# Performance work log

Measured on AMD Instinct MI355X. Metric: run time of the kernel, lower is better.

The kernel has to match this reference:

```python
import jax, jax.numpy as jnp
import numpy as np

N_NODES = 100000
N_EDGES = 1600000
IN_CH = 128
HIDDEN = 64
N_CLASSES = 40


def setup_inputs() -> dict:
    key = jax.random.key(0)
    k_x, k_e, k_w1, k_w2 = jax.random.split(key, 4)
    x = jax.random.normal(k_x, (N_NODES, IN_CH), dtype=jnp.float32)
    edge_index = jax.random.randint(k_e, (2, N_EDGES), 0, N_NODES, dtype=jnp.int64)
    # Glorot-style init for GCN weights
    W1 = jax.random.normal(k_w1, (IN_CH, HIDDEN), dtype=jnp.float32) * (1.0 / np.sqrt(IN_CH))
    b1 = jnp.zeros((HIDDEN,), dtype=jnp.float32)
    W2 = jax.random.normal(k_w2, (HIDDEN, N_CLASSES), dtype=jnp.float32) * (1.0 / np.sqrt(HIDDEN))
    b2 = jnp.zeros((N_CLASSES,), dtype=jnp.float32)
    return {"x": x, "edge_index": edge_index, "W1": W1, "b1": b1, "W2": W2, "b2": b2}


def reference(x, edge_index, W1, b1, W2, b2):
    n = x.shape[0]
    # PyG GCNConv: add self-loops, symmetric degree normalization
    loop = jnp.arange(n, dtype=edge_index.dtype)
    src = jnp.concatenate([edge_index[0], loop])  # message sources j
    dst = jnp.concatenate([edge_index[1], loop])  # aggregation targets i
    w = jnp.ones(src.shape[0], dtype=x.dtype)     # edge_weight=None -> ones
    deg = jax.ops.segment_sum(w, dst, num_segments=n)
    dinv = jnp.where(deg > 0, jax.lax.rsqrt(jnp.maximum(deg, 1e-12)), 0.0)
    norm = dinv[src] * dinv[dst]                  # [E+N]

    def gcn_conv(h, W, b):
        hw = h @ W                                # transform first (fewer flops)
        msg = hw[src] * norm[:, None]             # gather + normalize
        return jax.ops.segment_sum(msg, dst, num_segments=n) + b  # scatter-add

    h = jax.nn.relu(gcn_conv(x, W1, b1))
    # dropout is identity in eval mode
    out = gcn_conv(h, W2, b2)
    return out
```

## Files before the change

kernel.cpp:

```cpp
#include <hip/hip_runtime.h>
#include <hip/hip_bf16.h>

#define NNODES 100000
#define NEDGES 1600000
#define IN_CH 128
#define HID 64
#define NC 40
#define NPAD 100352
#define NBUK 196
#define CAP 9216
#define BCHUNK 4096
#define NBIN 391

typedef unsigned short ushort_t;
typedef unsigned int uint_t;
typedef __attribute__((ext_vector_type(8))) short short8;
typedef __attribute__((ext_vector_type(4))) float floatx4;
typedef __attribute__((ext_vector_type(2))) float f32x2;

__device__ __forceinline__ ushort_t f2bf(float f) {
    union { float ff; unsigned int i; } t;
    t.ff = f;
    unsigned int r = t.i + 0x7fff + ((t.i >> 16) & 1);
    return (ushort_t)(r >> 16);
}
__device__ __forceinline__ void acc2(f32x2& a, uint_t p) {
    union { unsigned int i; float f; } lo, hi;
    lo.i = p << 16;
    hi.i = p & 0xffff0000u;
    f32x2 v = {lo.f, hi.f};
    a += v;
}

__global__ __launch_bounds__(256) void k_bin0(
    const int* __restrict__ srcs, const int* __restrict__ dsts,
    int* __restrict__ gcur, uint_t* __restrict__ tmp, int e,
    const float* __restrict__ W1, ushort_t* __restrict__ Wp,
    ushort_t* __restrict__ hb, int n)
{
    __shared__ uint_t pk[BCHUNK];
    __shared__ ushort_t bk[BCHUNK];
    __shared__ uint_t spk[BCHUNK];
    __shared__ ushort_t sb[BCHUNK];
    __shared__ int hist[NBUK];
    __shared__ int lscan[NBUK];
    __shared__ int base[NBUK];
    __shared__ int sc2[256];
    int t = threadIdx.x;
    if (blockIdx.x >= NBIN) {
        for (int i = t; i < IN_CH * HID; i += 256) {
            int j = i & 7;
            int m = (i >> 3) & 15;
            int ct = (i >> 7) & 3;
            int quad = (i >> 9) & 3;
            int kc = i >> 11;
            int k = kc * 32 + quad * 8 + j;
            int c = ct * 16 + m;
            Wp[i] = f2bf(W1[k * HID + c]);
        }
        uint_t* hbz = (uint_t*)(hb + (size_t)n * HID);
        if (t < 32) hbz[t] = 0;
        return;
    }
    int begin = blockIdx.x * BCHUNK;
    int cnt = e - begin; if (cnt > BCHUNK) cnt = BCHUNK;

    for (int i = t; i < NBUK; i += 256) hist[i] = 0;
    __syncthreads();
    for (int j = t; j < cnt; j += 256) {
        int d = dsts[begin + j];
        int s = srcs[begin + j];
        int b = d >> 9;
        pk[j] = (uint_t)s | ((uint_t)(d & 511) << 17);
        bk[j] = (ushort_t)b;
        atomicAdd(&hist[b], 1);
    }
    __syncthreads();
    int c = (t < NBUK) ? hist[t] : 0;
    sc2[t] = c;
    __syncthreads();
    for (int off = 1; off < 256; off <<= 1) {
        int v = (t >= off) ? sc2[t - off] : 0;
        __syncthreads();
        sc2[t] += v;
        __syncthreads();
    }
    if (t < NBUK) {
        lscan[t] = sc2[t] - c;
        base[t] = t * CAP + atomicAdd(&gcur[t], c);
        hist[t] = 0;
    }
    __syncthreads();
    for (int j = t; j < cnt; j += 256) {
        int b = bk[j];
        int r = atomicAdd(&hist[b], 1);
        int slot = lscan[b] + r;
        spk[slot] = pk[j];
        sb[slot] = (ushort_t)b;
    }
    __syncthreads();
    for (int j = t; j < cnt; j += 256) {
        int b = sb[j];
        int pos = base[b] + (j - lscan[b]);
        if (pos < (b + 1) * CAP) tmp[pos] = spk[j];
    }
}

__global__ __launch_bounds__(256) void k_sort(
    const uint_t* __restrict__ tmp, const int* __restrict__ gcur,
    int* __restrict__ row_start, float* __restrict__ dinv,
    uint_t* __restrict__ es, int n, int e)
{
    __shared__ int cnt[512];
    __shared__ int sc[512];
    __shared__ int red[256];
    __shared__ uint_t esl[CAP];
    int t = threadIdx.x;
    int b = blockIdx.x;
    int d0 = b << 9;
    int total = gcur[b];
    if (total > CAP) total = CAP;
    int part = 0;
    for (int i = t; i < b; i += 256) part += gcur[i];
    red[t] = part;
    cnt[t] = 0; cnt[t + 256] = 0;
    __syncthreads();
    for (int off = 128; off > 0; off >>= 1) {
        if (t < off) red[t] += red[t + off];
        __syncthreads();
    }
    int gb = red[0];
    const uint_t* seg = tmp + b * CAP;
    for (int j = t; j < total; j += 256)
        atomicAdd(&cnt[seg[j] >> 17], 1);
    __syncthreads();
    sc[t] = cnt[t]; sc[t + 256] = cnt[t + 256];
    __syncthreads();
    for (int off = 1; off < 512; off <<= 1) {
        int v0 = (t >= off) ? sc[t - off] : 0;
        int i1 = t + 256;
        int v1 = (i1 >= off) ? sc[i1 - off] : 0;
        __syncthreads();
        sc[t] += v0; sc[i1] += v1;
        __syncthreads();
    }
#pragma unroll
    for (int q = 0; q < 2; ++q) {
        int i = t + q * 256;
        int node = d0 + i;
        int start = gb + sc[i] - cnt[i];
        if (node < n) {
            row_start[node] = start;
            dinv[node] = rsqrtf((float)cnt[i] + 1.0f);
        }
        cnt[i] = start - gb;
    }
    __syncthreads();
    for (int j = t; j < total; j += 256) {
        uint_t p = seg[j];
        int ld = (int)(p >> 17);
        int pos = atomicAdd(&cnt[ld], 1);
        esl[pos] = p & 0x1FFFFu;
    }
    __syncthreads();
    for (int j = t; j < total; j += 256) es[gb + j] = esl[j];
    if (b == NBUK - 1 && t == 0) row_start[n] = e;
}

__global__ __launch_bounds__(256) void k_gemm1(
    const float* __restrict__ x, const ushort_t* __restrict__ Wp,
    const float* __restrict__ dinv, ushort_t* __restrict__ hw1, int n)
{
    int wave = threadIdx.x >> 6;
    int lane = threadIdx.x & 63;
    int m = lane & 15;
    int quad = lane >> 4;
    int row = blockIdx.x * 64 + wave * 16 + m;
    int rowc = row < n ? row : (n - 1);
    const float* xr = x + (size_t)rowc * IN_CH + quad * 8;

    floatx4 acc[4];
#pragma unroll
    for (int ct = 0; ct < 4; ++ct) acc[ct] = (floatx4){0.f, 0.f, 0.f, 0.f};

#pragma unroll
    for (int kc = 0; kc < 4; ++kc) {
        float4 xa = *(const float4*)(xr + kc * 32);
        float4 xb = *(const float4*)(xr + kc * 32 + 4);
        short8 a;
        a[0] = (short)f2bf(xa.x); a[1] = (short)f2bf(xa.y);
        a[2] = (short)f2bf(xa.z); a[3] = (short)f2bf(xa.w);
        a[4] = (short)f2bf(xb.x); a[5] = (short)f2bf(xb.y);
        a[6] = (short)f2bf(xb.z); a[7] = (short)f2bf(xb.w);
#pragma unroll
        for (int ct = 0; ct < 4; ++ct) {
            short8 b = *(const short8*)(Wp + ((((kc * 4 + quad) * 4 + ct) * 16 + m) << 3));
            acc[ct] = __builtin_amdgcn_mfma_f32_16x16x32_bf16(a, b, acc[ct], 0, 0, 0);
        }
    }
    int r0 = blockIdx.x * 64 + wave * 16 + quad * 4;
#pragma unroll
    for (int r = 0; r < 4; ++r) {
        int rr = r0 + r;
        if (rr < n) {
            float di = dinv[rr];
            ushort_t* o = hw1 + (size_t)rr * HID + m;
#pragma unroll
            for (int ct = 0; ct < 4; ++ct) o[ct * 16] = f2bf(acc[ct][r] * di);
        } else if (rr == n) {
            ushort_t* o = hw1 + (size_t)n * HID + m;
#pragma unroll
            for (int ct = 0; ct < 4; ++ct) o[ct * 16] = 0;
        }
    }
}

__global__ __launch_bounds__(256, 4) void k_agg1(
    const int* __restrict__ row_start, const uint_t* __restrict__ es,
    const float* __restrict__ dinv, const uint_t* __restrict__ hw1u,
    const float* __restrict__ b1, ushort_t* __restrict__ hb, int n)
{
    int lane = threadIdx.x & 63;
    int obase = lane & 56;
    int ol = lane & 7;
    int node = blockIdx.x * 32 + (threadIdx.x >> 3);
    bool valid = node < n;
    int rs = valid ? row_start[node] : 0;
    int re = valid ? row_start[node + 1] : 0;
    float di = valid ? dinv[node] : 0.f;
    int selfrow = valid ? node : n;

    f32x2 c0, c1, c2, c3;
    {
        uint4 sp = *(const uint4*)(hw1u + (size_t)selfrow * 32 + ol * 4);
        c0 = (f32x2){0.f, 0.f}; c1 = c0; c2 = c0; c3 = c0;
        acc2(c0, sp.x); acc2(c1, sp.y); acc2(c2, sp.z); acc2(c3, sp.w);
    }
    int el = n;
    if (rs < re) {
        int idx = rs + ol;
        el = (idx < re) ? (int)es[idx] : n;
    }
    for (int base = rs; base < re; base += 8) {
        int el_cur = el;
        int nb = base + 8;
        if (nb < re) {
            int idx = nb + ol;
            el = (idx < re) ? (int)es[idx] : n;
        }
        uint4 p[8];
#pragma unroll
        for (int b = 0; b < 8; ++b) {
            int s = __shfl(el_cur, obase + b);
            p[b] = *(const uint4*)(hw1u + (size_t)s * 32 + ol * 4);
        }
#pragma unroll
        for (int b = 0; b < 8; ++b) {
            acc2(c0, p[b].x); acc2(c1, p[b].y);
            acc2(c2, p[b].z); acc2(c3, p[b].w);
        }
    }
    if (valid) {
        float4 bb0 = ((const float4*)b1)[ol * 2];
        float4 bb1 = ((const float4*)b1)[ol * 2 + 1];
        float h0 = fmaxf(c0.x * di + bb0.x, 0.f);
        float h1 = fmaxf(c0.y * di + bb0.y, 0.f);
        float h2 = fmaxf(c1.x * di + bb0.z, 0.f);
        float h3 = fmaxf(c1.y * di + bb0.w, 0.f);
        float h4 = fmaxf(c2.x * di + bb1.x, 0.f);
        float h5 = fmaxf(c2.y * di + bb1.y, 0.f);
        float h6 = fmaxf(c3.x * di + bb1.z, 0.f);
        float h7 = fmaxf(c3.y * di + bb1.w, 0.f);
        uint4 st;
        st.x = (uint_t)f2bf(h0 * di) | ((uint_t)f2bf(h1 * di) << 16);
        st.y = (uint_t)f2bf(h2 * di) | ((uint_t)f2bf(h3 * di) << 16);
        st.z = (uint_t)f2bf(h4 * di) | ((uint_t)f2bf(h5 * di) << 16);
        st.w = (uint_t)f2bf(h6 * di) | ((uint_t)f2bf(h7 * di) << 16);
        *(uint4*)(hb + (size_t)node * HID + ol * 8) = st;
    }
}

__global__ __launch_bounds__(256, 4) void k_agg2(
    const int* __restrict__ row_start, const uint_t* __restrict__ es,
    const float* __restrict__ dinv, const uint_t* __restrict__ hbu,
    const float* __restrict__ W2, const float* __restrict__ b2,
    float* __restrict__ out, int n)
{
    __shared__ float wsm[HID * NC];
    __shared__ float hsm[32][68];
    for (int i = threadIdx.x; i < HID * NC; i += 256) wsm[i] = W2[i];
    __syncthreads();

    int lane = threadIdx.x & 63;
    int obase = lane & 56;
    int ol = lane & 7;
    int slot = threadIdx.x >> 3;
    int node = blockIdx.x * 32 + slot;
    bool valid = node < n;
    int rs = valid ? row_start[node] : 0;
    int re = valid ? row_start[node + 1] : 0;
    float di = valid ? dinv[node] : 0.f;
    int selfrow = valid ? node : n;

    f32x2 c0, c1, c2, c3;
    {
        uint4 sp = *(const uint4*)(hbu + (size_t)selfrow * 32 + ol * 4);
        c0 = (f32x2){0.f, 0.f}; c1 = c0; c2 = c0; c3 = c0;
        acc2(c0, sp.x); acc2(c1, sp.y); acc2(c2, sp.z); acc2(c3, sp.w);
    }
    int el = n;
    if (rs < re) {
        int idx = rs + ol;
        el = (idx < re) ? (int)es[idx] : n;
    }
    for (int base = rs; base < re; base += 8) {
        int el_cur = el;
        int nb = base + 8;
        if (nb < re) {
            int idx = nb + ol;
            el = (idx < re) ? (int)es[idx] : n;
        }
        uint4 p[8];
#pragma unroll
        for (int b = 0; b < 8; ++b) {
            int s = __shfl(el_cur, obase + b);
            p[b] = *(const uint4*)(hbu + (size_t)s * 32 + ol * 4);
        }
#pragma unroll
        for (int b = 0; b < 8; ++b) {
            acc2(c0, p[b].x); acc2(c1, p[b].y);
            acc2(c2, p[b].z); acc2(c3, p[b].w);
        }
    }
    {
        float4 g0, g1;
        g0.x = c0.x * di; g0.y = c0.y * di; g0.z = c1.x * di; g0.w = c1.y * di;
        g1.x = c2.x * di; g1.y = c2.y * di; g1.z = c3.x * di; g1.w = c3.y * di;
        *(float4*)&hsm[slot][ol * 8] = g0;
        *(float4*)&hsm[slot][ol * 8 + 4] = g1;
    }
    int w8 = (threadIdx.x >> 6) * 8;
    int qm = lane >> 4;
    int lq = lane & 15;
    int lw = (lq < 10) ? lq : 0;
    const float4* w4 = (const float4*)wsm;
#pragma unroll
    for (int pass = 0; pass < 2; ++pass) {
        int slot2 = w8 + pass * 4 + qm;
        int node2 = blockIdx.x * 32 + slot2;
        float4 acc = ((const float4*)b2)[lw];
#pragma unroll 4
        for (int k4 = 0; k4 < 16; ++k4) {
            float4 hk = *(const float4*)&hsm[slot2][k4 * 4];
            float4 w0 = w4[(k4 * 4 + 0) * 10 + lw];
            float4 w1 = w4[(k4 * 4 + 1) * 10 + lw];
            float4 w2 = w4[(k4 * 4 + 2) * 10 + lw];
            float4 w3 = w4[(k4 * 4 + 3) * 10 + lw];
            acc.x += hk.x * w0.x + hk.y * w1.x + hk.z * w2.x + hk.w * w3.x;
            acc.y += hk.x * w0.y + hk.y * w1.y + hk.z * w2.y + hk.w * w3.y;
            acc.z += hk.x * w0.z + hk.y * w1.z + hk.z * w2.z + hk.w * w3.z;
            acc.w += hk.x * w0.w + hk.y * w1.w + hk.z * w2.w + hk.w * w3.w;
        }
        if (node2 < n && lq < 10)
            *(float4*)(out + (size_t)node2 * NC + lq * 4) = acc;
    }
}

extern "C" void kernel_launch(void* const* d_in, const int* in_sizes, int n_in,
                              void* d_out, int out_size, void* d_ws, size_t ws_size,
                              hipStream_t stream) {
    const float* x  = (const float*)d_in[0];
    const int* edge = (const int*)d_in[1];
    const float* W1 = (const float*)d_in[2];
    const float* b1 = (const float*)d_in[3];
    const float* W2 = (const float*)d_in[4];
    const float* b2 = (const float*)d_in[5];
    float* out      = (float*)d_out;

    const int n = in_sizes[0] / IN_CH;
    const int e = in_sizes[1] / 2;
    const int* srcs = edge;
    const int* dsts = edge + e;

    int*      gcur      = (int*)d_ws;
    int*      row_start = gcur + 256;
    float*    dinv      = (float*)(row_start + NPAD);
    uint_t*   tmp       = (uint_t*)(dinv + NPAD);
    uint_t*   es        = tmp + (size_t)NBUK * CAP;
    ushort_t* Wp        = (ushort_t*)(es + NEDGES);
    ushort_t* hw1       = Wp + 8192;
    ushort_t* hb        = hw1 + (size_t)(NNODES + 1) * HID;

    hipMemsetAsync(gcur, 0, NBUK * sizeof(int), stream);
    k_bin0<<<NBIN + 1, 256, 0, stream>>>(srcs, dsts, gcur, tmp, e, W1, Wp, hb, n);
    k_sort<<<NBUK, 256, 0, stream>>>(tmp, gcur, row_start, dinv, es, n, e);
    k_gemm1<<<(n + 63) / 64, 256, 0, stream>>>(x, Wp, dinv, hw1, n);
    k_agg1<<<(n + 31) / 32, 256, 0, stream>>>(row_start, es, dinv, (const uint_t*)hw1, b1, hb, n);
    k_agg2<<<(n + 31) / 32, 256, 0, stream>>>(row_start, es, dinv, (const uint_t*)hb, W2, b2, out, n);
}
```

Before: 211.2 us.

## Fuse all GCN stages into one persistent cooperative kernel with grid syncs

Merges binning, bucket sort, GEMM1, and both aggregation stages into a single cooperative kernel of 1024 persistent blocks, separated by grid-wide barriers and sharing a unioned LDS buffer. The aim is to remove per-kernel launch gaps and tail drain between stages. The binning chunk size is reduced so the LDS union fits four blocks per CU. In exchange, the aggregation stages run with fewer resident blocks looping over tiles and pay grid-sync costs, with a fallback to the separate kernels if the cooperative launch fails.

```diff
diff --git a/kernel.cpp b/kernel.cpp
--- a/kernel.cpp
+++ b/kernel.cpp
@@ -1,5 +1,8 @@
 #include <hip/hip_runtime.h>
 #include <hip/hip_bf16.h>
+#include <hip/hip_cooperative_groups.h>
+
+namespace cg = cooperative_groups;
 
 #define NNODES 100000
 #define NEDGES 1600000
@@ -9,8 +12,8 @@
 #define NPAD 100352
 #define NBUK 196
 #define CAP 9216
-#define BCHUNK 4096
-#define NBIN 391
+#define BCH 2560
+#define GRID 1024
 
 typedef unsigned short ushort_t;
 typedef unsigned int uint_t;
@@ -32,157 +35,153 @@
     a += v;
 }
 
-__global__ __launch_bounds__(256) void k_bin0(
+struct SmBin {
+    uint_t pk[BCH]; ushort_t bk[BCH];
+    uint_t spk[BCH]; ushort_t sb[BCH];
+    int hist[NBUK]; int lscan[NBUK]; int base[NBUK]; int sc2[256];
+};
+struct SmSortScan { int sc[512]; int red[256]; };
+struct SmSort { int cnt[512]; union { SmSortScan s; uint_t esl[CAP]; } u; };
+struct SmG2 { float wsm[HID * NC]; float hsm[32][68]; };
+union Sm { SmBin bin; SmSort sort; SmG2 g2; };
+static_assert(sizeof(Sm) <= 39936, "LDS budget for 4 blocks/CU");
+
+
+__device__ __forceinline__ void side_work(const float* __restrict__ W1,
+                                          ushort_t* __restrict__ Wp,
+                                          ushort_t* __restrict__ hb, int n, int t) {
+    for (int i = t; i < IN_CH * HID; i += 256) {
+        int j = i & 7;
+        int m = (i >> 3) & 15;
+        int ct = (i >> 7) & 3;
+        int quad = (i >> 9) & 3;
+        int kc = i >> 11;
+        int k = kc * 32 + quad * 8 + j;
+        int c = ct * 16 + m;
+        Wp[i] = f2bf(W1[k * HID + c]);
+    }
+    uint_t* hbz = (uint_t*)(hb + (size_t)n * HID);
+    if (t < 32) hbz[t] = 0;
+}
+
+__device__ __forceinline__ void bin_chunk(SmBin& sm, int chunk,
     const int* __restrict__ srcs, const int* __restrict__ dsts,
-    int* __restrict__ gcur, uint_t* __restrict__ tmp, int e,
-    const float* __restrict__ W1, ushort_t* __restrict__ Wp,
-    ushort_t* __restrict__ hb, int n)
-{
-    __shared__ uint_t pk[BCHUNK];
-    __shared__ ushort_t bk[BCHUNK];
-    __shared__ uint_t spk[BCHUNK];
-    __shared__ ushort_t sb[BCHUNK];
-    __shared__ int hist[NBUK];
-    __shared__ int lscan[NBUK];
-    __shared__ int base[NBUK];
-    __shared__ int sc2[256];
-    int t = threadIdx.x;
-    if (blockIdx.x >= NBIN) {
-        for (int i = t; i < IN_CH * HID; i += 256) {
-            int j = i & 7;
-            int m = (i >> 3) & 15;
-            int ct = (i >> 7) & 3;
-            int quad = (i >> 9) & 3;
-            int kc = i >> 11;
-            int k = kc * 32 + quad * 8 + j;
-            int c = ct * 16 + m;
-            Wp[i] = f2bf(W1[k * HID + c]);
-        }
-        uint_t* hbz = (uint_t*)(hb + (size_t)n * HID);
-        if (t < 32) hbz[t] = 0;
-        return;
-    }
-    int begin = blockIdx.x * BCHUNK;
-    int cnt = e - begin; if (cnt > BCHUNK) cnt = BCHUNK;
-
-    for (int i = t; i < NBUK; i += 256) hist[i] = 0;
-    __syncthreads();
-    for (int j = t; j < cnt; j += 256) {
+    int* __restrict__ gcur, uint_t* __restrict__ tmp, int e, int t)
+{
+    int begin = chunk * BCH;
+    int ec = e - begin; if (ec > BCH) ec = BCH;
+    for (int i = t; i < NBUK; i += 256) sm.hist[i] = 0;
+    __syncthreads();
+    for (int j = t; j < ec; j += 256) {
         int d = dsts[begin + j];
         int s = srcs[begin + j];
         int b = d >> 9;
-        pk[j] = (uint_t)s | ((uint_t)(d & 511) << 17);
-        bk[j] = (ushort_t)b;
-        atomicAdd(&hist[b], 1);
-    }
-    __syncthreads();
-    int c = (t < NBUK) ? hist[t] : 0;
-    sc2[t] = c;
+        sm.pk[j] = (uint_t)s | ((uint_t)(d & 511) << 17);
+        sm.bk[j] = (ushort_t)b;
+        atomicAdd(&sm.hist[b], 1);
+    }
+    __syncthreads();
+    int c = (t < NBUK) ? sm.hist[t] : 0;
+    sm.sc2[t] = c;
     __syncthreads();
     for (int off = 1; off < 256; off <<= 1) {
-        int v = (t >= off) ? sc2[t - off] : 0;
+        int v = (t >= off) ? sm.sc2[t - off] : 0;
         __syncthreads();
-        sc2[t] += v;
+        sm.sc2[t] += v;
         __syncthreads();
     }
     if (t < NBUK) {
-        lscan[t] = sc2[t] - c;
-        base[t] = t * CAP + atomicAdd(&gcur[t], c);
-        hist[t] = 0;
-    }
-    __syncthreads();
-    for (int j = t; j < cnt; j += 256) {
-        int b = bk[j];
-        int r = atomicAdd(&hist[b], 1);
-        int slot = lscan[b] + r;
-        spk[slot] = pk[j];
-        sb[slot] = (ushort_t)b;
-    }
-    __syncthreads();
-    for (int j = t; j < cnt; j += 256) {
-        int b = sb[j];
-        int pos = base[b] + (j - lscan[b]);
-        if (pos < (b + 1) * CAP) tmp[pos] = spk[j];
-    }
-}
-
-__global__ __launch_bounds__(256) void k_sort(
+        sm.lscan[t] = sm.sc2[t] - c;
+        sm.base[t] = t * CAP + atomicAdd(&gcur[t], c);
+        sm.hist[t] = 0;
+    }
+    __syncthreads();
+    for (int j = t; j < ec; j += 256) {
+        int b = sm.bk[j];
+        int r = atomicAdd(&sm.hist[b], 1);
+        int slot = sm.lscan[b] + r;
+        sm.spk[slot] = sm.pk[j];
+        sm.sb[slot] = (ushort_t)b;
+    }
+    __syncthreads();
+    for (int j = t; j < ec; j += 256) {
+        int b = sm.sb[j];
+        int pos = sm.base[b] + (j - sm.lscan[b]);
+        if (pos < (b + 1) * CAP) tmp[pos] = sm.spk[j];
+    }
+    __syncthreads();
+}
+
+__device__ __forceinline__ void sort_bucket(SmSort& sm, int b,
     const uint_t* __restrict__ tmp, const int* __restrict__ gcur,
     int* __restrict__ row_start, float* __restrict__ dinv,
-    uint_t* __restrict__ es, int n, int e)
-{
-    __shared__ int cnt[512];
-    __shared__ int sc[512];
-    __shared__ int red[256];
-    __shared__ uint_t esl[CAP];
-    int t = threadIdx.x;
-    int b = blockIdx.x;
+    uint_t* __restrict__ es, int n, int e, int t)
+{
     int d0 = b << 9;
     int total = gcur[b];
     if (total > CAP) total = CAP;
     int part = 0;
     for (int i = t; i < b; i += 256) part += gcur[i];
-    red[t] = part;
-    cnt[t] = 0; cnt[t + 256] = 0;
+    sm.u.s.red[t] = part;
+    sm.cnt[t] = 0; sm.cnt[t + 256] = 0;
     __syncthreads();
     for (int off = 128; off > 0; off >>= 1) {
-        if (t < off) red[t] += red[t + off];
+        if (t < off) sm.u.s.red[t] += sm.u.s.red[t + off];
         __syncthreads();
     }
-    int gb = red[0];
+    int gb = sm.u.s.red[0];
     const uint_t* seg = tmp + b * CAP;
     for (int j = t; j < total; j += 256)
-        atomicAdd(&cnt[seg[j] >> 17], 1);
-    __syncthreads();
-    sc[t] = cnt[t]; sc[t + 256] = cnt[t + 256];
+        atomicAdd(&sm.cnt[seg[j] >> 17], 1);
+    __syncthreads();
+    sm.u.s.sc[t] = sm.cnt[t]; sm.u.s.sc[t + 256] = sm.cnt[t + 256];
     __syncthreads();
     for (int off = 1; off < 512; off <<= 1) {
-        int v0 = (t >= off) ? sc[t - off] : 0;
+        int v0 = (t >= off) ? sm.u.s.sc[t - off] : 0;
         int i1 = t + 256;
-        int v1 = (i1 >= off) ? sc[i1 - off] : 0;
+        int v1 = (i1 >= off) ? sm.u.s.sc[i1 - off] : 0;
         __syncthreads();
-        sc[t] += v0; sc[i1] += v1;
+        sm.u.s.sc[t] += v0; sm.u.s.sc[i1] += v1;
         __syncthreads();
     }
 #pragma unroll
     for (int q = 0; q < 2; ++q) {
         int i = t + q * 256;
         int node = d0 + i;
-        int start = gb + sc[i] - cnt[i];
+        int start = gb + sm.u.s.sc[i] - sm.cnt[i];
         if (node < n) {
             row_start[node] = start;
-            dinv[node] = rsqrtf((float)cnt[i] + 1.0f);
-        }
-        cnt[i] = start - gb;
+            dinv[node] = rsqrtf((float)sm.cnt[i] + 1.0f);
+        }
+        sm.cnt[i] = start - gb;
     }
     __syncthreads();
     for (int j = t; j < total; j += 256) {
         uint_t p = seg[j];
         int ld = (int)(p >> 17);
-        int pos = atomicAdd(&cnt[ld], 1);
-        esl[pos] = p & 0x1FFFFu;
-    }
-    __syncthreads();
-    for (int j = t; j < total; j += 256) es[gb + j] = esl[j];
+        int pos = atomicAdd(&sm.cnt[ld], 1);
+        sm.u.esl[pos] = p & 0x1FFFFu;
+    }
+    __syncthreads();
+    for (int j = t; j < total; j += 256) es[gb + j] = sm.u.esl[j];
     if (b == NBUK - 1 && t == 0) row_start[n] = e;
-}
-
-__global__ __launch_bounds__(256) void k_gemm1(
+    __syncthreads();
+}
+
+__device__ __forceinline__ void gemm1_tile(int g,
     const float* __restrict__ x, const ushort_t* __restrict__ Wp,
-    const float* __restrict__ dinv, ushort_t* __restrict__ hw1, int n)
-{
-    int wave = threadIdx.x >> 6;
-    int lane = threadIdx.x & 63;
+    const float* __restrict__ dinv, ushort_t* __restrict__ hw1, int n, int t)
+{
+    int wave = t >> 6;
+    int lane = t & 63;
     int m = lane & 15;
     int quad = lane >> 4;
-    int row = blockIdx.x * 64 + wave * 16 + m;
+    int row = g * 64 + wave * 16 + m;
     int rowc = row < n ? row : (n - 1);
     const float* xr = x + (size_t)rowc * IN_CH + quad * 8;
-
     floatx4 acc[4];
 #pragma unroll
     for (int ct = 0; ct < 4; ++ct) acc[ct] = (floatx4){0.f, 0.f, 0.f, 0.f};
-
 #pragma unroll
     for (int kc = 0; kc < 4; ++kc) {
         float4 xa = *(const float4*)(xr + kc * 32);
@@ -194,11 +193,11 @@
         a[6] = (short)f2bf(xb.z); a[7] = (short)f2bf(xb.w);
 #pragma unroll
         for (int ct = 0; ct < 4; ++ct) {
-            short8 b = *(const short8*)(Wp + ((((kc * 4 + quad) * 4 + ct) * 16 + m) << 3));
-            acc[ct] = __builtin_amdgcn_mfma_f32_16x16x32_bf16(a, b, acc[ct], 0, 0, 0);
-        }
-    }
-    int r0 = blockIdx.x * 64 + wave * 16 + quad * 4;
+            short8 bfr = *(const short8*)(Wp + ((((kc * 4 + quad) * 4 + ct) * 16 + m) << 3));
+            acc[ct] = __builtin_amdgcn_mfma_f32_16x16x32_bf16(a, bfr, acc[ct], 0, 0, 0);
+        }
+    }
+    int r0 = g * 64 + wave * 16 + quad * 4;
 #pragma unroll
     for (int r = 0; r < 4; ++r) {
         int rr = r0 + r;
@@ -215,21 +214,20 @@
     }
 }
 
-__global__ __launch_bounds__(256, 4) void k_agg1(
+__device__ __forceinline__ void agg1_tile(int g,
     const int* __restrict__ row_start, const uint_t* __restrict__ es,
     const float* __restrict__ dinv, const uint_t* __restrict__ hw1u,
-    const float* __restrict__ b1, ushort_t* __restrict__ hb, int n)
-{
-    int lane = threadIdx.x & 63;
+    const float* __restrict__ b1, ushort_t* __restrict__ hb, int n, int t)
+{
+    int lane = t & 63;
     int obase = lane & 56;
     int ol = lane & 7;
-    int node = blockIdx.x * 32 + (threadIdx.x >> 3);
+    int node = g * 32 + (t >> 3);
     bool valid = node < n;
     int rs = valid ? row_start[node] : 0;
     int re = valid ? row_start[node + 1] : 0;
     float di = valid ? dinv[node] : 0.f;
     int selfrow = valid ? node : n;
-
     f32x2 c0, c1, c2, c3;
     {
         uint4 sp = *(const uint4*)(hw1u + (size_t)selfrow * 32 + ol * 4);
@@ -280,28 +278,21 @@
     }
 }
 
-__global__ __launch_bounds__(256, 4) void k_agg2(
+__device__ __forceinline__ void agg2_tile(SmG2& sm, int g,
     const int* __restrict__ row_start, const uint_t* __restrict__ es,
     const float* __restrict__ dinv, const uint_t* __restrict__ hbu,
-    const float* __restrict__ W2, const float* __restrict__ b2,
-    float* __restrict__ out, int n)
-{
-    __shared__ float wsm[HID * NC];
-    __shared__ float hsm[32][68];
-    for (int i = threadIdx.x; i < HID * NC; i += 256) wsm[i] = W2[i];
-    __syncthreads();
-
-    int lane = threadIdx.x & 63;
+    const float* __restrict__ b2, float* __restrict__ out, int n, int t)
+{
+    int lane = t & 63;
     int obase = lane & 56;
     int ol = lane & 7;
-    int slot = threadIdx.x >> 3;
-    int node = blockIdx.x * 32 + slot;
+    int slot = t >> 3;
+    int node = g * 32 + slot;
     bool valid = node < n;
     int rs = valid ? row_start[node] : 0;
     int re = valid ? row_start[node + 1] : 0;
     float di = valid ? dinv[node] : 0.f;
     int selfrow = valid ? node : n;
-
     f32x2 c0, c1, c2, c3;
     {
         uint4 sp = *(const uint4*)(hbu + (size_t)selfrow * 32 + ol * 4);
@@ -336,22 +327,22 @@
         float4 g0, g1;
         g0.x = c0.x * di; g0.y = c0.y * di; g0.z = c1.x * di; g0.w = c1.y * di;
         g1.x = c2.x * di; g1.y = c2.y * di; g1.z = c3.x * di; g1.w = c3.y * di;
-        *(float4*)&hsm[slot][ol * 8] = g0;
-        *(float4*)&hsm[slot][ol * 8 + 4] = g1;
-    }
-    int w8 = (threadIdx.x >> 6) * 8;
+        *(float4*)&sm.hsm[slot][ol * 8] = g0;
+        *(float4*)&sm.hsm[slot][ol * 8 + 4] = g1;
+    }
+    int w8 = (t >> 6) * 8;
     int qm = lane >> 4;
     int lq = lane & 15;
     int lw = (lq < 10) ? lq : 0;
-    const float4* w4 = (const float4*)wsm;
+    const float4* w4 = (const float4*)sm.wsm;
 #pragma unroll
     for (int pass = 0; pass < 2; ++pass) {
         int slot2 = w8 + pass * 4 + qm;
-        int node2 = blockIdx.x * 32 + slot2;
+        int node2 = g * 32 + slot2;
         float4 acc = ((const float4*)b2)[lw];
 #pragma unroll 4
         for (int k4 = 0; k4 < 16; ++k4) {
-            float4 hk = *(const float4*)&hsm[slot2][k4 * 4];
+            float4 hk = *(const float4*)&sm.hsm[slot2][k4 * 4];
             float4 w0 = w4[(k4 * 4 + 0) * 10 + lw];
             float4 w1 = w4[(k4 * 4 + 1) * 10 + lw];
             float4 w2 = w4[(k4 * 4 + 2) * 10 + lw];
@@ -364,6 +355,105 @@
         if (node2 < n && lq < 10)
             *(float4*)(out + (size_t)node2 * NC + lq * 4) = acc;
     }
+}
+
+extern "C" __global__ void __launch_bounds__(256, 4) k_all(
+    const int* __restrict__ srcs, const int* __restrict__ dsts,
+    int* __restrict__ gcur, uint_t* __restrict__ tmp,
+    const float* __restrict__ W1, ushort_t* __restrict__ Wp,
+    ushort_t* __restrict__ hb,
+    int* __restrict__ row_start, float* __restrict__ dinv,
+    uint_t* __restrict__ es,
+    const float* __restrict__ x, ushort_t* __restrict__ hw1,
+    const float* __restrict__ b1,
+    const float* __restrict__ W2, const float* __restrict__ b2,
+    float* __restrict__ out, int n, int e)
+{
+    __shared__ Sm sm;
+    cg::grid_group grid = cg::this_grid();
+    int t = threadIdx.x;
+    int nchunk = (e + BCH - 1) / BCH;
+
+    if ((int)blockIdx.x == nchunk) side_work(W1, Wp, hb, n, t);
+    for (int chunk = blockIdx.x; chunk < nchunk; chunk += GRID)
+        bin_chunk(sm.bin, chunk, srcs, dsts, gcur, tmp, e, t);
+    grid.sync();
+
+    for (int b = blockIdx.x; b < NBUK; b += GRID)
+        sort_bucket(sm.sort, b, tmp, gcur, row_start, dinv, es, n, e, t);
+    grid.sync();
+
+    {
+        int ng = (n + 63) >> 6;
+        for (int g = blockIdx.x; g < ng; g += GRID)
+            gemm1_tile(g, x, Wp, dinv, hw1, n, t);
+    }
+    grid.sync();
+
+    {
+        const uint_t* hw1u = (const uint_t*)hw1;
+        int nga = (n + 31) >> 5;
+        for (int g = blockIdx.x; g < nga; g += GRID)
+            agg1_tile(g, row_start, es, dinv, hw1u, b1, hb, n, t);
+    }
+    grid.sync();
+
+    {
+        const uint_t* hbu = (const uint_t*)hb;
+        for (int i = t; i < HID * NC; i += 256) sm.g2.wsm[i] = W2[i];
+        __syncthreads();
+        int nga = (n + 31) >> 5;
+        for (int g = blockIdx.x; g < nga; g += GRID)
+            agg2_tile(sm.g2, g, row_start, es, dinv, hbu, b2, out, n, t);
+    }
+}
+
+__global__ __launch_bounds__(256) void k_bin0(
+    const int* __restrict__ srcs, const int* __restrict__ dsts,
+    int* __restrict__ gcur, uint_t* __restrict__ tmp, int e,
+    const float* __restrict__ W1, ushort_t* __restrict__ Wp,
+    ushort_t* __restrict__ hb, int n)
+{
+    __shared__ SmBin smb;
+    int nchunk = (e + BCH - 1) / BCH;
+    if ((int)blockIdx.x >= nchunk) { side_work(W1, Wp, hb, n, threadIdx.x); return; }
+    bin_chunk(smb, blockIdx.x, srcs, dsts, gcur, tmp, e, threadIdx.x);
+}
+
+__global__ __launch_bounds__(256) void k_sort(
+    const uint_t* __restrict__ tmp, const int* __restrict__ gcur,
+    int* __restrict__ row_start, float* __restrict__ dinv,
+    uint_t* __restrict__ es, int n, int e)
+{
+    __shared__ SmSort sms;
+    sort_bucket(sms, blockIdx.x, tmp, gcur, row_start, dinv, es, n, e, threadIdx.x);
+}
+
+__global__ __launch_bounds__(256) void k_gemm1(
+    const float* __restrict__ x, const ushort_t* __restrict__ Wp,
+    const float* __restrict__ dinv, ushort_t* __restrict__ hw1, int n)
+{
+    gemm1_tile(blockIdx.x, x, Wp, dinv, hw1, n, threadIdx.x);
+}
+
+__global__ __launch_bounds__(256, 4) void k_agg1(
+    const int* __restrict__ row_start, const uint_t* __restrict__ es,
+    const float* __restrict__ dinv, const uint_t* __restrict__ hw1u,
+    const float* __restrict__ b1, ushort_t* __restrict__ hb, int n)
+{
+    agg1_tile(blockIdx.x, row_start, es, dinv, hw1u, b1, hb, n, threadIdx.x);
+}
+
+__global__ __launch_bounds__(256, 4) void k_agg2(
+    const int* __restrict__ row_start, const uint_t* __restrict__ es,
+    const float* __restrict__ dinv, const uint_t* __restrict__ hbu,
+    const float* __restrict__ W2, const float* __restrict__ b2,
+    float* __restrict__ out, int n)
+{
+    __shared__ SmG2 smg;
+    for (int i = threadIdx.x; i < HID * NC; i += 256) smg.wsm[i] = W2[i];
+    __syncthreads();
+    agg2_tile(smg, blockIdx.x, row_start, es, dinv, hbu, b2, out, n, threadIdx.x);
 }
 
 extern "C" void kernel_launch(void* const* d_in, const int* in_sizes, int n_in,
@@ -377,8 +467,8 @@
     const float* b2 = (const float*)d_in[5];
     float* out      = (float*)d_out;
 
-    const int n = in_sizes[0] / IN_CH;
-    const int e = in_sizes[1] / 2;
+    int n = in_sizes[0] / IN_CH;
+    int e = in_sizes[1] / 2;
     const int* srcs = edge;
     const int* dsts = edge + e;
 
@@ -391,10 +481,25 @@
     ushort_t* hw1       = Wp + 8192;
     ushort_t* hb        = hw1 + (size_t)(NNODES + 1) * HID;
 
-    hipMemsetAsync(gcur, 0, NBUK * sizeof(int), stream);
-    k_bin0<<<NBIN + 1, 256, 0, stream>>>(srcs, dsts, gcur, tmp, e, W1, Wp, hb, n);
-    k_sort<<<NBUK, 256, 0, stream>>>(tmp, gcur, row_start, dinv, es, n, e);
-    k_gemm1<<<(n + 63) / 64, 256, 0, stream>>>(x, Wp, dinv, hw1, n);
-    k_agg1<<<(n + 31) / 32, 256, 0, stream>>>(row_start, es, dinv, (const uint_t*)hw1, b1, hb, n);
-    k_agg2<<<(n + 31) / 32, 256, 0, stream>>>(row_start, es, dinv, (const uint_t*)hb, W2, b2, out, n);
-}
+    hipMemsetAsync(gcur, 0, 256 * sizeof(int), stream);
+
+    void* args[] = {
+        (void*)&srcs, (void*)&dsts, (void*)&gcur, (void*)&tmp,
+        (void*)&W1, (void*)&Wp, (void*)&hb,
+        (void*)&row_start, (void*)&dinv, (void*)&es,
+        (void*)&x, (void*)&hw1, (void*)&b1,
+        (void*)&W2, (void*)&b2, (void*)&out,
+        (void*)&n, (void*)&e
+    };
+    hipError_t err = hipLaunchCooperativeKernel((void*)k_all, dim3(GRID), dim3(256),
+                                                args, 0, stream);
+    if (err != hipSuccess) {
+        (void)hipGetLastError();
+        int nchunk = (e + BCH - 1) / BCH;
+        k_bin0<<<nchunk + 1, 256, 0, stream>>>(srcs, dsts, gcur, tmp, e, W1, Wp, hb, n);
+        k_sort<<<NBUK, 256, 0, stream>>>(tmp, gcur, row_start, dinv, es, n, e);
+        k_gemm1<<<(n + 63) / 64, 256, 0, stream>>>(x, Wp, dinv, hw1, n);
+        k_agg1<<<(n + 31) / 32, 256, 0, stream>>>(row_start, es, dinv, (const uint_t*)hw1, b1, hb, n);
+        k_agg2<<<(n + 31) / 32, 256, 0, stream>>>(row_start, es, dinv, (const uint_t*)hb, W2, b2, out, n);
+    }
+}
```

New measurement: 698.0 us. 3.3x slower.

## Fuse layer-1 GEMM into binning kernel, apply source dinv during aggregation

Applied to the files above, without the earlier changes.

Moves the X·W1 MFMA GEMM into extra blocks of the binning kernel so it runs concurrently with edge binning instead of after the sort. Each GEMM block repacks W1 into shared memory itself, so no global staging buffer is needed. Because dinv is not known at that point, the GEMM output is left unscaled. agg1 now gathers dinv[src] per edge and multiplies it in, which costs extra gathers and FMAs in the aggregation loop. It also adjusts row_start/dinv writes for padded nodes and drops the separate row_start[n] write.

```diff
diff --git a/kernel.cpp b/kernel.cpp
--- a/kernel.cpp
+++ b/kernel.cpp
@@ -24,6 +24,13 @@
     unsigned int r = t.i + 0x7fff + ((t.i >> 16) & 1);
     return (ushort_t)(r >> 16);
 }
+__device__ __forceinline__ void acc2w(f32x2& a, uint_t p, float w) {
+    union { unsigned int i; float f; } lo, hi;
+    lo.i = p << 16;
+    hi.i = p & 0xffff0000u;
+    a.x += lo.f * w;
+    a.y += hi.f * w;
+}
 __device__ __forceinline__ void acc2(f32x2& a, uint_t p) {
     union { unsigned int i; float f; } lo, hi;
     lo.i = p << 16;
@@ -32,11 +39,11 @@
     a += v;
 }
 
-__global__ __launch_bounds__(256) void k_bin0(
+__global__ __launch_bounds__(256) void k_bg(
     const int* __restrict__ srcs, const int* __restrict__ dsts,
     int* __restrict__ gcur, uint_t* __restrict__ tmp, int e,
-    const float* __restrict__ W1, ushort_t* __restrict__ Wp,
-    ushort_t* __restrict__ hb, int n)
+    const float* __restrict__ W1, ushort_t* __restrict__ hb,
+    const float* __restrict__ x, ushort_t* __restrict__ hw1, int n)
 {
     __shared__ uint_t pk[BCHUNK];
     __shared__ ushort_t bk[BCHUNK];
@@ -47,7 +54,9 @@
     __shared__ int base[NBUK];
     __shared__ int sc2[256];
     int t = threadIdx.x;
-    if (blockIdx.x >= NBIN) {
+
+    if ((int)blockIdx.x > NBIN) {
+        ushort_t* wl = (ushort_t*)pk;
         for (int i = t; i < IN_CH * HID; i += 256) {
             int j = i & 7;
             int m = (i >> 3) & 15;
@@ -56,15 +65,58 @@
             int kc = i >> 11;
             int k = kc * 32 + quad * 8 + j;
             int c = ct * 16 + m;
-            Wp[i] = f2bf(W1[k * HID + c]);
-        }
+            wl[i] = f2bf(W1[k * HID + c]);
+        }
+        __syncthreads();
+        int blk = blockIdx.x - (NBIN + 1);
+        int wave = t >> 6;
+        int lane = t & 63;
+        int m = lane & 15;
+        int quad = lane >> 4;
+        int row = blk * 64 + wave * 16 + m;
+        int rowc = row < n ? row : (n - 1);
+        const float* xr = x + (size_t)rowc * IN_CH + quad * 8;
+        floatx4 acc[4];
+#pragma unroll
+        for (int ct = 0; ct < 4; ++ct) acc[ct] = (floatx4){0.f, 0.f, 0.f, 0.f};
+#pragma unroll
+        for (int kc = 0; kc < 4; ++kc) {
+            float4 xa = *(const float4*)(xr + kc * 32);
+            float4 xb = *(const float4*)(xr + kc * 32 + 4);
+            short8 a;
+            a[0] = (short)f2bf(xa.x); a[1] = (short)f2bf(xa.y);
+            a[2] = (short)f2bf(xa.z); a[3] = (short)f2bf(xa.w);
+            a[4] = (short)f2bf(xb.x); a[5] = (short)f2bf(xb.y);
+            a[6] = (short)f2bf(xb.z); a[7] = (short)f2bf(xb.w);
+#pragma unroll
+            for (int ct = 0; ct < 4; ++ct) {
+                short8 bfr = *(const short8*)(wl + ((((kc * 4 + quad) * 4 + ct) * 16 + m) << 3));
+                acc[ct] = __builtin_amdgcn_mfma_f32_16x16x32_bf16(a, bfr, acc[ct], 0, 0, 0);
+            }
+        }
+        int r0 = blk * 64 + wave * 16 + quad * 4;
+#pragma unroll
+        for (int r = 0; r < 4; ++r) {
+            int rr = r0 + r;
+            if (rr < n) {
+                ushort_t* o = hw1 + (size_t)rr * HID + m;
+#pragma unroll
+                for (int ct = 0; ct < 4; ++ct) o[ct * 16] = f2bf(acc[ct][r]);
+            } else if (rr == n) {
+                ushort_t* o = hw1 + (size_t)n * HID + m;
+#pragma unroll
+                for (int ct = 0; ct < 4; ++ct) o[ct * 16] = 0;
+            }
+        }
+        return;
+    }
+    if ((int)blockIdx.x == NBIN) {
         uint_t* hbz = (uint_t*)(hb + (size_t)n * HID);
         if (t < 32) hbz[t] = 0;
         return;
     }
     int begin = blockIdx.x * BCHUNK;
     int cnt = e - begin; if (cnt > BCHUNK) cnt = BCHUNK;
-
     for (int i = t; i < NBUK; i += 256) hist[i] = 0;
     __syncthreads();
     for (int j = t; j < cnt; j += 256) {
@@ -149,10 +201,8 @@
         int i = t + q * 256;
         int node = d0 + i;
         int start = gb + sc[i] - cnt[i];
-        if (node < n) {
-            row_start[node] = start;
-            dinv[node] = rsqrtf((float)cnt[i] + 1.0f);
-        }
+        row_start[node] = start;
+        dinv[node] = (node < n) ? rsqrtf((float)cnt[i] + 1.0f) : 0.f;
         cnt[i] = start - gb;
     }
     __syncthreads();
@@ -164,55 +214,6 @@
     }
     __syncthreads();
     for (int j = t; j < total; j += 256) es[gb + j] = esl[j];
-    if (b == NBUK - 1 && t == 0) row_start[n] = e;
-}
-
-__global__ __launch_bounds__(256) void k_gemm1(
-    const float* __restrict__ x, const ushort_t* __restrict__ Wp,
-    const float* __restrict__ dinv, ushort_t* __restrict__ hw1, int n)
-{
-    int wave = threadIdx.x >> 6;
-    int lane = threadIdx.x & 63;
-    int m = lane & 15;
-    int quad = lane >> 4;
-    int row = blockIdx.x * 64 + wave * 16 + m;
-    int rowc = row < n ? row : (n - 1);
-    const float* xr = x + (size_t)rowc * IN_CH + quad * 8;
-
-    floatx4 acc[4];
-#pragma unroll
-    for (int ct = 0; ct < 4; ++ct) acc[ct] = (floatx4){0.f, 0.f, 0.f, 0.f};
-
-#pragma unroll
-    for (int kc = 0; kc < 4; ++kc) {
-        float4 xa = *(const float4*)(xr + kc * 32);
-        float4 xb = *(const float4*)(xr + kc * 32 + 4);
-        short8 a;
-        a[0] = (short)f2bf(xa.x); a[1] = (short)f2bf(xa.y);
-        a[2] = (short)f2bf(xa.z); a[3] = (short)f2bf(xa.w);
-        a[4] = (short)f2bf(xb.x); a[5] = (short)f2bf(xb.y);
-        a[6] = (short)f2bf(xb.z); a[7] = (short)f2bf(xb.w);
-#pragma unroll
-        for (int ct = 0; ct < 4; ++ct) {
-            short8 b = *(const short8*)(Wp + ((((kc * 4 + quad) * 4 + ct) * 16 + m) << 3));
-            acc[ct] = __builtin_amdgcn_mfma_f32_16x16x32_bf16(a, b, acc[ct], 0, 0, 0);
-        }
-    }
-    int r0 = blockIdx.x * 64 + wave * 16 + quad * 4;
-#pragma unroll
-    for (int r = 0; r < 4; ++r) {
-        int rr = r0 + r;
-        if (rr < n) {
-            float di = dinv[rr];
-            ushort_t* o = hw1 + (size_t)rr * HID + m;
-#pragma unroll
-            for (int ct = 0; ct < 4; ++ct) o[ct * 16] = f2bf(acc[ct][r] * di);
-        } else if (rr == n) {
-            ushort_t* o = hw1 + (size_t)n * HID + m;
-#pragma unroll
-            for (int ct = 0; ct < 4; ++ct) o[ct * 16] = 0;
-        }
-    }
 }
 
 __global__ __launch_bounds__(256, 4) void k_agg1(
@@ -234,30 +235,34 @@
     {
         uint4 sp = *(const uint4*)(hw1u + (size_t)selfrow * 32 + ol * 4);
         c0 = (f32x2){0.f, 0.f}; c1 = c0; c2 = c0; c3 = c0;
-        acc2(c0, sp.x); acc2(c1, sp.y); acc2(c2, sp.z); acc2(c3, sp.w);
-    }
-    int el = n;
+        acc2w(c0, sp.x, di); acc2w(c1, sp.y, di);
+        acc2w(c2, sp.z, di); acc2w(c3, sp.w, di);
+    }
+    int el = n; float dv = 0.f;
     if (rs < re) {
         int idx = rs + ol;
         el = (idx < re) ? (int)es[idx] : n;
+        dv = dinv[el];
     }
     for (int base = rs; base < re; base += 8) {
-        int el_cur = el;
+        int el_cur = el; float dv_cur = dv;
         int nb = base + 8;
         if (nb < re) {
             int idx = nb + ol;
             el = (idx < re) ? (int)es[idx] : n;
-        }
-        uint4 p[8];
+            dv = dinv[el];
+        }
+        uint4 p[8]; float w[8];
 #pragma unroll
         for (int b = 0; b < 8; ++b) {
             int s = __shfl(el_cur, obase + b);
+            w[b] = __shfl(dv_cur, obase + b);
             p[b] = *(const uint4*)(hw1u + (size_t)s * 32 + ol * 4);
         }
 #pragma unroll
         for (int b = 0; b < 8; ++b) {
-            acc2(c0, p[b].x); acc2(c1, p[b].y);
-            acc2(c2, p[b].z); acc2(c3, p[b].w);
+            acc2w(c0, p[b].x, w[b]); acc2w(c1, p[b].y, w[b]);
+            acc2w(c2, p[b].z, w[b]); acc2w(c3, p[b].w, w[b]);
         }
     }
     if (valid) {
@@ -387,14 +392,14 @@
     float*    dinv      = (float*)(row_start + NPAD);
     uint_t*   tmp       = (uint_t*)(dinv + NPAD);
     uint_t*   es        = tmp + (size_t)NBUK * CAP;
-    ushort_t* Wp        = (ushort_t*)(es + NEDGES);
-    ushort_t* hw1       = Wp + 8192;
+    ushort_t* hw1       = (ushort_t*)(es + NEDGES);
     ushort_t* hb        = hw1 + (size_t)(NNODES + 1) * HID;
 
+    const int ng1 = (n + 63) / 64;
+
     hipMemsetAsync(gcur, 0, NBUK * sizeof(int), stream);
-    k_bin0<<<NBIN + 1, 256, 0, stream>>>(srcs, dsts, gcur, tmp, e, W1, Wp, hb, n);
+    k_bg<<<NBIN + 1 + ng1, 256, 0, stream>>>(srcs, dsts, gcur, tmp, e, W1, hb, x, hw1, n);
     k_sort<<<NBUK, 256, 0, stream>>>(tmp, gcur, row_start, dinv, es, n, e);
-    k_gemm1<<<(n + 63) / 64, 256, 0, stream>>>(x, Wp, dinv, hw1, n);
     k_agg1<<<(n + 31) / 32, 256, 0, stream>>>(row_start, es, dinv, (const uint_t*)hw1, b1, hb, n);
     k_agg2<<<(n + 31) / 32, 256, 0, stream>>>(row_start, es, dinv, (const uint_t*)hb, W2, b2, out, n);
 }
```

After: 214.4 us. No clear change (+1.5%).
